# Kernel tuning notes

Measured on AMD Instinct MI355X. Metric: run time of the kernel, lower is better.

The kernel has to match this reference:

```python
import jax, jax.numpy as jnp
import numpy as np

N = 1024
EMB = 128
FC = 512


def setup_inputs() -> dict:
    key = jax.random.key(0)
    ks = jax.random.split(key, 13)
    s = 0.05
    return {
        "x": jax.random.normal(ks[0], (N, 2), jnp.float32),
        "w_rel0": jax.random.normal(ks[1], (EMB, 2), jnp.float32) * s,
        "b_rel0": jax.random.normal(ks[2], (EMB,), jnp.float32) * s,
        "w_root0": jax.random.normal(ks[3], (EMB, 2), jnp.float32) * s,
        "w_rel1": jax.random.normal(ks[4], (EMB, EMB), jnp.float32) * s,
        "b_rel1": jax.random.normal(ks[5], (EMB,), jnp.float32) * s,
        "w_root1": jax.random.normal(ks[6], (EMB, EMB), jnp.float32) * s,
        "lw0": jax.random.normal(ks[7], (FC, EMB), jnp.float32) * s,
        "lb0": jax.random.normal(ks[8], (FC,), jnp.float32) * s,
        "lw1": jax.random.normal(ks[9], (FC, FC), jnp.float32) * s,
        "lb1": jax.random.normal(ks[10], (FC,), jnp.float32) * s,
        "lw2": jax.random.normal(ks[11], (1, FC), jnp.float32) * s,
        "lb2": jax.random.normal(ks[12], (1,), jnp.float32) * s,
    }


def _sage(x, w_rel, b_rel, w_root):
    # DenseSAGEConv with adj = all-ones NxN: neighbor mean == global mean.
    # out = lin_rel(adj@x / deg) + lin_root(x); lin_root has no bias.
    agg = jnp.mean(x, axis=0, keepdims=True)            # (1, d_in)
    return agg @ w_rel.T + b_rel + x @ w_root.T          # (N, d_out)


def reference(x, w_rel0, b_rel0, w_root0, w_rel1, b_rel1, w_root1,
              lw0, lb0, lw1, lb1, lw2, lb2):
    h = jax.nn.relu(_sage(x, w_rel0, b_rel0, w_root0))    # (N, EMB)
    h = jax.nn.relu(_sage(h, w_rel1, b_rel1, w_root1))    # (N, EMB)
    # triu(ones, 1).nonzero() -> all pairs i < j (static, N known at trace time)
    ei, ej = np.triu_indices(h.shape[0], 1)
    e = h[ei] * h[ej]                                     # (E, EMB)
    o = jax.nn.relu(e @ lw0.T + lb0)                      # (E, FC)
    o = jax.nn.relu(o @ lw1.T + lb1)                      # (E, FC)
    o = o @ lw2.T + lb2                                   # (E, 1)
    return jax.nn.sigmoid(o)[:, 0]                        # (E,)
```

## Files before the change

### kernel.cpp

```cpp
#include <hip/hip_runtime.h>
#include <hip/hip_bf16.h>
#include <math.h>

#define NN 1024
#define EMB 128
#define FC 512
#define NEDGE 523776
#define BM 64

typedef __attribute__((ext_vector_type(4))) float f32x4;
typedef __attribute__((ext_vector_type(8))) short bf16x8;
typedef __attribute__((ext_vector_type(4))) unsigned int u32x4;
typedef __attribute__((ext_vector_type(8))) int i32x8;

__device__ __forceinline__ float bf2f(unsigned short u) {
  union { unsigned int i; float f; } v; v.i = ((unsigned int)u) << 16; return v.f;
}
__device__ __forceinline__ unsigned short f2bf(float f) {
  return __builtin_bit_cast(unsigned short, __float2bfloat16(f));
}
__device__ __forceinline__ int cum_edges(int i) { return i * NN - ((i * (i + 1)) >> 1); }

__device__ __forceinline__ unsigned int pk4_fp8(float a, float b, float c, float d) {
  int v = __builtin_amdgcn_cvt_pk_fp8_f32(a, b, 0, false);
  v = __builtin_amdgcn_cvt_pk_fp8_f32(c, d, v, true);
  return (unsigned int)v;
}
#define MFMA_FP8_L0(A,B,C) __builtin_amdgcn_mfma_scale_f32_16x16x128_f8f6f4((A),(B),(C),0,0,0,0x76767676,0,0x7f7f7f7f)
#define MFMA_FP8_L1(A,B,C) __builtin_amdgcn_mfma_scale_f32_16x16x128_f8f6f4((A),(B),(C),0,0,0,0x72727272,0,0x7f7f7f7f)

__global__ void k_cvt_weights(const float* __restrict__ lw0, const float* __restrict__ lw1,
                              unsigned int* __restrict__ w0q, unsigned int* __restrict__ w1q) {
  int d = blockIdx.x * 256 + threadIdx.x;
  if (d < 16384) {
    int dw = d & 7, lane = (d >> 3) & 63, f = (d >> 9) & 3, wv = d >> 11;
    int fc = wv*64 + f*16 + (lane & 15);
    int k  = (lane >> 4)*32 + dw*4;
    float4 s = *(const float4*)(lw0 + fc*EMB + k);
    w0q[d] = pk4_fp8(s.x*64.f, s.y*64.f, s.z*64.f, s.w*64.f);
  } else {
    int u = d - 16384;
    int dw = u & 7, lane = (u >> 3) & 63, f = (u >> 9) & 3, kb = (u >> 11) & 3, wv = u >> 13;
    int fc = wv*64 + f*16 + (lane & 15);
    int k  = kb*128 + (lane >> 4)*32 + dw*4;
    float4 s = *(const float4*)(lw1 + fc*FC + k);
    w1q[u] = pk4_fp8(s.x*64.f, s.y*64.f, s.z*64.f, s.w*64.f);
  }
}

__global__ void k_mean_x(const float* __restrict__ x, float* __restrict__ mean0) {
  __shared__ float sx[256], sy[256];
  float ax = 0.f, ay = 0.f;
  for (int i = threadIdx.x; i < NN; i += 256) { ax += x[2*i]; ay += x[2*i+1]; }
  sx[threadIdx.x] = ax; sy[threadIdx.x] = ay;
  __syncthreads();
  for (int st = 128; st > 0; st >>= 1) {
    if (threadIdx.x < st) { sx[threadIdx.x] += sx[threadIdx.x+st]; sy[threadIdx.x] += sy[threadIdx.x+st]; }
    __syncthreads();
  }
  if (threadIdx.x == 0) { mean0[0] = sx[0] * (1.f/NN); mean0[1] = sy[0] * (1.f/NN); }
}

__global__ void k_sage0(const float* __restrict__ x, const float* __restrict__ wrel,
                        const float* __restrict__ brel, const float* __restrict__ wroot,
                        const float* __restrict__ mean0, float* __restrict__ h0) {
  int idx = blockIdx.x * 256 + threadIdx.x;
  int i = idx >> 7, c = idx & 127;
  float v = mean0[0]*wrel[2*c] + mean0[1]*wrel[2*c+1] + brel[c]
          + x[2*i]*wroot[2*c] + x[2*i+1]*wroot[2*c+1];
  h0[idx] = fmaxf(v, 0.f);
}

__global__ void k_mean_h0(const float* __restrict__ h0, float* __restrict__ mean1) {
  __shared__ float s[256];
  int c = blockIdx.x;
  float a = 0.f;
  for (int i = threadIdx.x; i < NN; i += 256) a += h0[i*EMB + c];
  s[threadIdx.x] = a;
  __syncthreads();
  for (int st = 128; st > 0; st >>= 1) {
    if (threadIdx.x < st) s[threadIdx.x] += s[threadIdx.x+st];
    __syncthreads();
  }
  if (threadIdx.x == 0) mean1[c] = s[0] * (1.f/NN);
}

__global__ void k_relc(const float* __restrict__ mean1, const float* __restrict__ wrel1,
                       const float* __restrict__ brel1, float* __restrict__ relc) {
  int c = threadIdx.x;
  float a = brel1[c];
  #pragma unroll 8
  for (int k = 0; k < EMB; ++k) a += mean1[k] * wrel1[c*EMB + k];
  relc[c] = a;
}

__global__ void k_sage1(const float* __restrict__ h0, const float* __restrict__ wroot1,
                        const float* __restrict__ relc, unsigned short* __restrict__ hb) {
  int idx = blockIdx.x * 256 + threadIdx.x;
  int i = idx >> 7, c = idx & 127;
  const float4* hr = (const float4*)(h0 + i*EMB);
  const float4* wr = (const float4*)(wroot1 + c*EMB);
  float a = relc[c];
  #pragma unroll 8
  for (int k = 0; k < EMB/4; ++k) {
    float4 h = hr[k], w = wr[k];
    a += h.x*w.x + h.y*w.y + h.z*w.z + h.w*w.w;
  }
  hb[idx] = f2bf(fmaxf(a, 0.f) * 32.0f);
}

__global__ __launch_bounds__(512, 4)
void k_edge_mlp(const unsigned short* __restrict__ hb,
                const unsigned int* __restrict__ w0q,
                const float* __restrict__ lb0,
                const unsigned int* __restrict__ w1q,
                const float* __restrict__ lb1,
                const float* __restrict__ lw2,
                const float* __restrict__ lb2,
                float* __restrict__ out) {
  __shared__ __align__(16) unsigned int e_lds[2048];
  __shared__ __align__(16) unsigned int o0_lds[8192];

  const int tid  = threadIdx.x;
  const int lane = tid & 63;
  const int wv   = tid >> 6;
  const int l15  = lane & 15;
  const int l4   = lane >> 4;
  const int blk  = blockIdx.x;
  const int fcb  = wv * 64;

  const char* w0w = (const char*)(w0q + wv * 2048);
  const char* w1w = (const char*)(w1q + wv * 8192);

  {
    int r = tid >> 3, q = tid & 7;
    int k = blk * BM + r;
    float s = sqrtf((float)(4190209 - 8*k));
    int i = (int)((2047.0f - s) * 0.5f);
    if (i < 0) i = 0;
    if (i > NN-2) i = NN-2;
    if (cum_edges(i+1) <= k) ++i;
    if (cum_edges(i+1) <= k) ++i;
    if (cum_edges(i) > k) --i;
    if (cum_edges(i) > k) --i;
    int j = k - cum_edges(i) + i + 1;
    const bf16x8* hi = (const bf16x8*)(hb + i*EMB + q*16);
    const bf16x8* hj = (const bf16x8*)(hb + j*EMB + q*16);
    float p[16];
    #pragma unroll
    for (int g = 0; g < 2; ++g) {
      bf16x8 a = hi[g], b = hj[g];
      #pragma unroll
      for (int u = 0; u < 8; ++u)
        p[g*8+u] = bf2f((unsigned short)a[u]) * bf2f((unsigned short)b[u]);
    }
    u32x4 d;
    #pragma unroll
    for (int u = 0; u < 4; ++u)
      d[u] = pk4_fp8(p[4*u], p[4*u+1], p[4*u+2], p[4*u+3]);
    int byt = (r>>4)*2048 + (q&1)*1024 + ((q>>1)*16 + (r&15))*16;
    *(u32x4*)((char*)e_lds + byt) = d;
  }
  __syncthreads();

  i32x8 a[4];
  #pragma unroll
  for (int f = 0; f < 4; ++f) {
    *(u32x4*)&a[f]       = *(const u32x4*)(w0w + f*2048 + lane*32);
    *((u32x4*)&a[f] + 1) = *(const u32x4*)(w0w + f*2048 + lane*32 + 16);
  }
  f32x4 acc[4][4];
  #pragma unroll
  for (int f = 0; f < 4; ++f) {
    float4 bv = *(const float4*)(lb0 + fcb + f*16 + l4*4);
    #pragma unroll
    for (int e = 0; e < 4; ++e)
      acc[e][f] = (f32x4){bv.x*128.f, bv.y*128.f, bv.z*128.f, bv.w*128.f};
  }
  {
    const char* rbe = (const char*)e_lds + lane*16;
    #pragma unroll
    for (int e = 0; e < 4; ++e) {
      i32x8 b;
      *(u32x4*)&b       = *(const u32x4*)(rbe + e*2048);
      *((u32x4*)&b + 1) = *(const u32x4*)(rbe + e*2048 + 1024);
      __builtin_amdgcn_s_setprio(1);
      #pragma unroll
      for (int f = 0; f < 4; ++f)
        acc[e][f] = MFMA_FP8_L0(a[f], b, acc[e][f]);
      __builtin_amdgcn_s_setprio(0);
    }
  }

  {
    char* ob = (char*)o0_lds + (wv>>1)*2048 + (wv&1)*512 + l15*16 + l4*4;
    #pragma unroll
    for (int f = 0; f < 4; ++f) {
      #pragma unroll
      for (int e = 0; e < 4; ++e) {
        unsigned int d = pk4_fp8(fmaxf(acc[e][f][0], 0.f),
                                 fmaxf(acc[e][f][1], 0.f),
                                 fmaxf(acc[e][f][2], 0.f),
                                 fmaxf(acc[e][f][3], 0.f));
        *(unsigned int*)(ob + e*8192 + (f&1)*1024 + (f>>1)*256) = d;
      }
    }
  }
  __syncthreads();

  #pragma unroll
  for (int f = 0; f < 4; ++f) {
    float4 bv = *(const float4*)(lb1 + fcb + f*16 + l4*4);
    #pragma unroll
    for (int e = 0; e < 4; ++e)
      acc[e][f] = (f32x4){bv.x, bv.y, bv.z, bv.w};
  }
  {
    const char* rbo = (const char*)o0_lds + lane*16;
    #pragma unroll
    for (int kb = 0; kb < 4; ++kb) {
      #pragma unroll
      for (int f = 0; f < 4; ++f) {
        *(u32x4*)&a[f]       = *(const u32x4*)(w1w + kb*8192 + f*2048 + lane*32);
        *((u32x4*)&a[f] + 1) = *(const u32x4*)(w1w + kb*8192 + f*2048 + lane*32 + 16);
      }
      #pragma unroll
      for (int e = 0; e < 4; ++e) {
        i32x8 b;
        *(u32x4*)&b       = *(const u32x4*)(rbo + e*8192 + kb*2048);
        *((u32x4*)&b + 1) = *(const u32x4*)(rbo + e*8192 + kb*2048 + 1024);
        __builtin_amdgcn_s_setprio(1);
        #pragma unroll
        for (int f = 0; f < 4; ++f)
          acc[e][f] = MFMA_FP8_L1(a[f], b, acc[e][f]);
        __builtin_amdgcn_s_setprio(0);
      }
    }
  }

  {
    float rs[4] = {0.f, 0.f, 0.f, 0.f};
    #pragma unroll
    for (int f = 0; f < 4; ++f) {
      float4 l2v = *(const float4*)(lw2 + fcb + f*16 + l4*4);
      #pragma unroll
      for (int e = 0; e < 4; ++e) {
        rs[e] += fmaxf(acc[e][f][0], 0.f) * l2v.x;
        rs[e] += fmaxf(acc[e][f][1], 0.f) * l2v.y;
        rs[e] += fmaxf(acc[e][f][2], 0.f) * l2v.z;
        rs[e] += fmaxf(acc[e][f][3], 0.f) * l2v.w;
      }
    }
    #pragma unroll
    for (int e = 0; e < 4; ++e) {
      rs[e] += __shfl_xor(rs[e], 16, 64);
      rs[e] += __shfl_xor(rs[e], 32, 64);
    }
    float* red = (float*)e_lds;
    if (l4 == 0) {
      #pragma unroll
      for (int e = 0; e < 4; ++e) red[wv*BM + e*16 + l15] = rs[e];
    }
  }
  __syncthreads();

  if (tid < BM) {
    const float* red = (const float*)e_lds;
    float v = lb2[0];
    #pragma unroll
    for (int w = 0; w < 8; ++w) v += red[w*BM + tid];
    out[blk*BM + tid] = 1.0f / (1.0f + __expf(-v));
  }
}

extern "C" void kernel_launch(void* const* d_in, const int* in_sizes, int n_in,
                              void* d_out, int out_size, void* d_ws, size_t ws_size,
                              hipStream_t stream) {
  const float* x      = (const float*)d_in[0];
  const float* wrel0  = (const float*)d_in[1];
  const float* brel0  = (const float*)d_in[2];
  const float* wroot0 = (const float*)d_in[3];
  const float* wrel1  = (const float*)d_in[4];
  const float* brel1  = (const float*)d_in[5];
  const float* wroot1 = (const float*)d_in[6];
  const float* lw0    = (const float*)d_in[7];
  const float* lb0    = (const float*)d_in[8];
  const float* lw1    = (const float*)d_in[9];
  const float* lb1    = (const float*)d_in[10];
  const float* lw2    = (const float*)d_in[11];
  const float* lb2    = (const float*)d_in[12];
  float* out = (float*)d_out;

  char* ws = (char*)d_ws;
  unsigned short* hb  = (unsigned short*)(ws);
  unsigned int*   w0q = (unsigned int*)(ws + 262144);
  unsigned int*   w1q = (unsigned int*)(ws + 327680);
  float* h0    = (float*)(ws + 589824);
  float* mean0 = (float*)(ws + 1114112);
  float* mean1 = (float*)(ws + 1114176);
  float* relc  = (float*)(ws + 1114688);

  hipLaunchKernelGGL(k_cvt_weights, dim3(320), dim3(256), 0, stream, lw0, lw1, w0q, w1q);
  hipLaunchKernelGGL(k_mean_x,   dim3(1),    dim3(256), 0, stream, x, mean0);
  hipLaunchKernelGGL(k_sage0,    dim3(512),  dim3(256), 0, stream, x, wrel0, brel0, wroot0, mean0, h0);
  hipLaunchKernelGGL(k_mean_h0,  dim3(128),  dim3(256), 0, stream, h0, mean1);
  hipLaunchKernelGGL(k_relc,     dim3(1),    dim3(128), 0, stream, mean1, wrel1, brel1, relc);
  hipLaunchKernelGGL(k_sage1,    dim3(512),  dim3(256), 0, stream, h0, wroot1, relc, hb);
  hipLaunchKernelGGL(k_edge_mlp, dim3(NEDGE/BM), dim3(512), 0, stream,
                     hb, w0q, lb0, w1q, lb1, lw2, lb2, out);
}
```

Baseline: 218.2 us.

## Double-buffer layer-1 weight fragments and split edges into two accumulator halves

```diff
diff --git a/kernel.cpp b/kernel.cpp
--- a/kernel.cpp
+++ b/kernel.cpp
@@ -109,6 +109,46 @@
   hb[idx] = f2bf(fmaxf(a, 0.f) * 32.0f);
 }
 
+
+#define L1_PRE(BUF, KB) \
+  { _Pragma("unroll") \
+    for (int f = 0; f < 4; ++f) { \
+      *(u32x4*)&BUF[f]       = *(const u32x4*)(w1w + (KB)*8192 + f*2048 + lane*32); \
+      *((u32x4*)&BUF[f] + 1) = *(const u32x4*)(w1w + (KB)*8192 + f*2048 + lane*32 + 16); \
+    } }
+
+#define L1_MM(BUF, KB, ET0, ET1) \
+  { i32x8 bA, bB; \
+    *(u32x4*)&bA       = *(const u32x4*)(rbo + (ET0)*8192 + (KB)*2048); \
+    *((u32x4*)&bA + 1) = *(const u32x4*)(rbo + (ET0)*8192 + (KB)*2048 + 1024); \
+    *(u32x4*)&bB       = *(const u32x4*)(rbo + (ET1)*8192 + (KB)*2048); \
+    *((u32x4*)&bB + 1) = *(const u32x4*)(rbo + (ET1)*8192 + (KB)*2048 + 1024); \
+    __builtin_amdgcn_s_setprio(1); \
+    _Pragma("unroll") \
+    for (int f = 0; f < 4; ++f) acc1[0][f] = MFMA_FP8_L1(BUF[f], bA, acc1[0][f]); \
+    _Pragma("unroll") \
+    for (int f = 0; f < 4; ++f) acc1[1][f] = MFMA_FP8_L1(BUF[f], bB, acc1[1][f]); \
+    __builtin_amdgcn_s_setprio(0); }
+
+#define L1_EPI(E0, E1) \
+  { float rs0 = 0.f, rs1 = 0.f; \
+    _Pragma("unroll") \
+    for (int f = 0; f < 4; ++f) { \
+      float4 bv  = *(const float4*)(lb1 + fcb + f*16 + l4*4); \
+      float4 wv2 = *(const float4*)(lw2 + fcb + f*16 + l4*4); \
+      rs0 += fmaxf(acc1[0][f][0] + bv.x, 0.f) * wv2.x; \
+      rs0 += fmaxf(acc1[0][f][1] + bv.y, 0.f) * wv2.y; \
+      rs0 += fmaxf(acc1[0][f][2] + bv.z, 0.f) * wv2.z; \
+      rs0 += fmaxf(acc1[0][f][3] + bv.w, 0.f) * wv2.w; \
+      rs1 += fmaxf(acc1[1][f][0] + bv.x, 0.f) * wv2.x; \
+      rs1 += fmaxf(acc1[1][f][1] + bv.y, 0.f) * wv2.y; \
+      rs1 += fmaxf(acc1[1][f][2] + bv.z, 0.f) * wv2.z; \
+      rs1 += fmaxf(acc1[1][f][3] + bv.w, 0.f) * wv2.w; \
+    } \
+    rs0 += __shfl_xor(rs0, 16, 64); rs0 += __shfl_xor(rs0, 32, 64); \
+    rs1 += __shfl_xor(rs1, 16, 64); rs1 += __shfl_xor(rs1, 32, 64); \
+    if (l4 == 0) { red[wv*64 + (E0)*16 + l15] = rs0; red[wv*64 + (E1)*16 + l15] = rs1; } }
+
 __global__ __launch_bounds__(512, 4)
 void k_edge_mlp(const unsigned short* __restrict__ hb,
                 const unsigned int* __restrict__ w0q,
@@ -131,6 +171,16 @@
 
   const char* w0w = (const char*)(w0q + wv * 2048);
   const char* w1w = (const char*)(w1q + wv * 8192);
+
+  i32x8 a0[4], a1[4];
+  #pragma unroll
+  for (int f = 0; f < 4; ++f) {
+    *(u32x4*)&a0[f]       = *(const u32x4*)(w0w + f*2048 + lane*32);
+    *((u32x4*)&a0[f] + 1) = *(const u32x4*)(w0w + f*2048 + lane*32 + 16);
+  }
+  float4 b0v[4];
+  #pragma unroll
+  for (int f = 0; f < 4; ++f) b0v[f] = *(const float4*)(lb0 + fcb + f*16 + l4*4);
 
   {
     int r = tid >> 3, q = tid & 7;
@@ -163,36 +213,30 @@
   }
   __syncthreads();
 
-  i32x8 a[4];
-  #pragma unroll
-  for (int f = 0; f < 4; ++f) {
-    *(u32x4*)&a[f]       = *(const u32x4*)(w0w + f*2048 + lane*32);
-    *((u32x4*)&a[f] + 1) = *(const u32x4*)(w0w + f*2048 + lane*32 + 16);
-  }
-  f32x4 acc[4][4];
-  #pragma unroll
-  for (int f = 0; f < 4; ++f) {
-    float4 bv = *(const float4*)(lb0 + fcb + f*16 + l4*4);
-    #pragma unroll
-    for (int e = 0; e < 4; ++e)
-      acc[e][f] = (f32x4){bv.x*128.f, bv.y*128.f, bv.z*128.f, bv.w*128.f};
-  }
   {
-    const char* rbe = (const char*)e_lds + lane*16;
-    #pragma unroll
-    for (int e = 0; e < 4; ++e) {
-      i32x8 b;
-      *(u32x4*)&b       = *(const u32x4*)(rbe + e*2048);
-      *((u32x4*)&b + 1) = *(const u32x4*)(rbe + e*2048 + 1024);
-      __builtin_amdgcn_s_setprio(1);
+    f32x4 acc[4][4];
+    #pragma unroll
+    for (int f = 0; f < 4; ++f)
       #pragma unroll
-      for (int f = 0; f < 4; ++f)
-        acc[e][f] = MFMA_FP8_L0(a[f], b, acc[e][f]);
-      __builtin_amdgcn_s_setprio(0);
+      for (int e = 0; e < 4; ++e)
+        acc[e][f] = (f32x4){b0v[f].x*128.f, b0v[f].y*128.f, b0v[f].z*128.f, b0v[f].w*128.f};
+    {
+      const char* rbe = (const char*)e_lds + lane*16;
+      #pragma unroll
+      for (int e = 0; e < 4; ++e) {
+        i32x8 b;
+        *(u32x4*)&b       = *(const u32x4*)(rbe + e*2048);
+        *((u32x4*)&b + 1) = *(const u32x4*)(rbe + e*2048 + 1024);
+        __builtin_amdgcn_s_setprio(1);
+        #pragma unroll
+        for (int f = 0; f < 4; ++f)
+          acc[e][f] = MFMA_FP8_L0(a0[f], b, acc[e][f]);
+        __builtin_amdgcn_s_setprio(0);
+      }
     }
-  }
-
-  {
+
+    L1_PRE(a0, 0);
+
     char* ob = (char*)o0_lds + (wv>>1)*2048 + (wv&1)*512 + l15*16 + l4*4;
     #pragma unroll
     for (int f = 0; f < 4; ++f) {
@@ -208,64 +252,34 @@
   }
   __syncthreads();
 
+  const char* rbo = (const char*)o0_lds + lane*16;
+  float* red = (float*)e_lds;
+  f32x4 acc1[2][4];
+
   #pragma unroll
-  for (int f = 0; f < 4; ++f) {
-    float4 bv = *(const float4*)(lb1 + fcb + f*16 + l4*4);
-    #pragma unroll
-    for (int e = 0; e < 4; ++e)
-      acc[e][f] = (f32x4){bv.x, bv.y, bv.z, bv.w};
-  }
-  {
-    const char* rbo = (const char*)o0_lds + lane*16;
-    #pragma unroll
-    for (int kb = 0; kb < 4; ++kb) {
-      #pragma unroll
-      for (int f = 0; f < 4; ++f) {
-        *(u32x4*)&a[f]       = *(const u32x4*)(w1w + kb*8192 + f*2048 + lane*32);
-        *((u32x4*)&a[f] + 1) = *(const u32x4*)(w1w + kb*8192 + f*2048 + lane*32 + 16);
-      }
-      #pragma unroll
-      for (int e = 0; e < 4; ++e) {
-        i32x8 b;
-        *(u32x4*)&b       = *(const u32x4*)(rbo + e*8192 + kb*2048);
-        *((u32x4*)&b + 1) = *(const u32x4*)(rbo + e*8192 + kb*2048 + 1024);
-        __builtin_amdgcn_s_setprio(1);
-        #pragma unroll
-        for (int f = 0; f < 4; ++f)
-          acc[e][f] = MFMA_FP8_L1(a[f], b, acc[e][f]);
-        __builtin_amdgcn_s_setprio(0);
-      }
-    }
-  }
-
-  {
-    float rs[4] = {0.f, 0.f, 0.f, 0.f};
-    #pragma unroll
-    for (int f = 0; f < 4; ++f) {
-      float4 l2v = *(const float4*)(lw2 + fcb + f*16 + l4*4);
-      #pragma unroll
-      for (int e = 0; e < 4; ++e) {
-        rs[e] += fmaxf(acc[e][f][0], 0.f) * l2v.x;
-        rs[e] += fmaxf(acc[e][f][1], 0.f) * l2v.y;
-        rs[e] += fmaxf(acc[e][f][2], 0.f) * l2v.z;
-        rs[e] += fmaxf(acc[e][f][3], 0.f) * l2v.w;
-      }
-    }
-    #pragma unroll
-    for (int e = 0; e < 4; ++e) {
-      rs[e] += __shfl_xor(rs[e], 16, 64);
-      rs[e] += __shfl_xor(rs[e], 32, 64);
-    }
-    float* red = (float*)e_lds;
-    if (l4 == 0) {
-      #pragma unroll
-      for (int e = 0; e < 4; ++e) red[wv*BM + e*16 + l15] = rs[e];
-    }
-  }
+  for (int p = 0; p < 2; ++p)
+    #pragma unroll
+    for (int f = 0; f < 4; ++f)
+      acc1[p][f] = (f32x4){0.f, 0.f, 0.f, 0.f};
+  L1_PRE(a1, 1);  L1_MM(a0, 0, 0, 1);
+  L1_PRE(a0, 2);  L1_MM(a1, 1, 0, 1);
+  L1_PRE(a1, 3);  L1_MM(a0, 2, 0, 1);
+                  L1_MM(a1, 3, 0, 1);
+  L1_EPI(0, 1);
+
+  #pragma unroll
+  for (int p = 0; p < 2; ++p)
+    #pragma unroll
+    for (int f = 0; f < 4; ++f)
+      acc1[p][f] = (f32x4){0.f, 0.f, 0.f, 0.f};
+  L1_PRE(a0, 2);  L1_MM(a1, 3, 2, 3);
+  L1_PRE(a1, 1);  L1_MM(a0, 2, 2, 3);
+  L1_PRE(a0, 0);  L1_MM(a1, 1, 2, 3);
+                  L1_MM(a0, 0, 2, 3);
+  L1_EPI(2, 3);
   __syncthreads();
 
   if (tid < BM) {
-    const float* red = (const float*)e_lds;
     float v = lb2[0];
     #pragma unroll
     for (int w = 0; w < 8; ++w) v += red[w*BM + tid];
```

Result: slower. 357.7 us (+63.9%).

## Switch edge MLP from 16x16x128 to 32x32x64 FP8 scaled MFMA tiles

Applied to the files above, without the earlier changes.

```diff
diff --git a/kernel.cpp b/kernel.cpp
--- a/kernel.cpp
+++ b/kernel.cpp
@@ -8,7 +8,7 @@
 #define NEDGE 523776
 #define BM 64
 
-typedef __attribute__((ext_vector_type(4))) float f32x4;
+typedef __attribute__((ext_vector_type(16))) float f32x16;
 typedef __attribute__((ext_vector_type(8))) short bf16x8;
 typedef __attribute__((ext_vector_type(4))) unsigned int u32x4;
 typedef __attribute__((ext_vector_type(8))) int i32x8;
@@ -26,23 +26,23 @@
   v = __builtin_amdgcn_cvt_pk_fp8_f32(c, d, v, true);
   return (unsigned int)v;
 }
-#define MFMA_FP8_L0(A,B,C) __builtin_amdgcn_mfma_scale_f32_16x16x128_f8f6f4((A),(B),(C),0,0,0,0x76767676,0,0x7f7f7f7f)
-#define MFMA_FP8_L1(A,B,C) __builtin_amdgcn_mfma_scale_f32_16x16x128_f8f6f4((A),(B),(C),0,0,0,0x72727272,0,0x7f7f7f7f)
+#define MFMA32_L0(A,B,C) __builtin_amdgcn_mfma_scale_f32_32x32x64_f8f6f4((A),(B),(C),0,0,0,0x76767676,0,0x7f7f7f7f)
+#define MFMA32_L1(A,B,C) __builtin_amdgcn_mfma_scale_f32_32x32x64_f8f6f4((A),(B),(C),0,0,0,0x72727272,0,0x7f7f7f7f)
 
 __global__ void k_cvt_weights(const float* __restrict__ lw0, const float* __restrict__ lw1,
                               unsigned int* __restrict__ w0q, unsigned int* __restrict__ w1q) {
   int d = blockIdx.x * 256 + threadIdx.x;
   if (d < 16384) {
-    int dw = d & 7, lane = (d >> 3) & 63, f = (d >> 9) & 3, wv = d >> 11;
-    int fc = wv*64 + f*16 + (lane & 15);
-    int k  = (lane >> 4)*32 + dw*4;
+    int dw = d & 7, lane = (d >> 3) & 63, f = (d >> 9) & 1, kb = (d >> 10) & 1, wv = (d >> 11) & 7;
+    int fc = wv*64 + f*32 + (lane & 31);
+    int k  = kb*64 + (lane >> 5)*32 + dw*4;
     float4 s = *(const float4*)(lw0 + fc*EMB + k);
     w0q[d] = pk4_fp8(s.x*64.f, s.y*64.f, s.z*64.f, s.w*64.f);
   } else {
     int u = d - 16384;
-    int dw = u & 7, lane = (u >> 3) & 63, f = (u >> 9) & 3, kb = (u >> 11) & 3, wv = u >> 13;
-    int fc = wv*64 + f*16 + (lane & 15);
-    int k  = kb*128 + (lane >> 4)*32 + dw*4;
+    int dw = u & 7, lane = (u >> 3) & 63, f = (u >> 9) & 1, kb = (u >> 10) & 7, wv = (u >> 13) & 7;
+    int fc = wv*64 + f*32 + (lane & 31);
+    int k  = kb*64 + (lane >> 5)*32 + dw*4;
     float4 s = *(const float4*)(lw1 + fc*FC + k);
     w1q[u] = pk4_fp8(s.x*64.f, s.y*64.f, s.z*64.f, s.w*64.f);
   }
@@ -118,19 +118,19 @@
                 const float* __restrict__ lw2,
                 const float* __restrict__ lb2,
                 float* __restrict__ out) {
-  __shared__ __align__(16) unsigned int e_lds[2048];
-  __shared__ __align__(16) unsigned int o0_lds[8192];
+  __shared__ __align__(32) unsigned int e_lds[2048];
+  __shared__ __align__(32) unsigned int o0_lds[8192];
 
   const int tid  = threadIdx.x;
   const int lane = tid & 63;
   const int wv   = tid >> 6;
-  const int l15  = lane & 15;
-  const int l4   = lane >> 4;
+  const int l31  = lane & 31;
+  const int hi   = lane >> 5;
   const int blk  = blockIdx.x;
   const int fcb  = wv * 64;
 
-  const char* w0w = (const char*)(w0q + wv * 2048);
-  const char* w1w = (const char*)(w1q + wv * 8192);
+  const char* w0w = (const char*)w0q + wv * 8192;
+  const char* w1w = (const char*)w1q + wv * 32768;
 
   {
     int r = tid >> 3, q = tid & 7;
@@ -144,12 +144,12 @@
     if (cum_edges(i) > k) --i;
     if (cum_edges(i) > k) --i;
     int j = k - cum_edges(i) + i + 1;
-    const bf16x8* hi = (const bf16x8*)(hb + i*EMB + q*16);
-    const bf16x8* hj = (const bf16x8*)(hb + j*EMB + q*16);
+    const bf16x8* hi8 = (const bf16x8*)(hb + i*EMB + q*16);
+    const bf16x8* hj8 = (const bf16x8*)(hb + j*EMB + q*16);
     float p[16];
     #pragma unroll
     for (int g = 0; g < 2; ++g) {
-      bf16x8 a = hi[g], b = hj[g];
+      bf16x8 a = hi8[g], b = hj8[g];
       #pragma unroll
       for (int u = 0; u < 8; ++u)
         p[g*8+u] = bf2f((unsigned short)a[u]) * bf2f((unsigned short)b[u]);
@@ -158,108 +158,108 @@
     #pragma unroll
     for (int u = 0; u < 4; ++u)
       d[u] = pk4_fp8(p[4*u], p[4*u+1], p[4*u+2], p[4*u+3]);
-    int byt = (r>>4)*2048 + (q&1)*1024 + ((q>>1)*16 + (r&15))*16;
+    int byt = (r>>5)*4096 + (q>>2)*2048 + ((q>>1)&1)*1024 + (r&31)*32 + (q&1)*16;
     *(u32x4*)((char*)e_lds + byt) = d;
   }
   __syncthreads();
 
-  i32x8 a[4];
+  f32x16 acc[2][2];
+
   #pragma unroll
-  for (int f = 0; f < 4; ++f) {
-    *(u32x4*)&a[f]       = *(const u32x4*)(w0w + f*2048 + lane*32);
-    *((u32x4*)&a[f] + 1) = *(const u32x4*)(w0w + f*2048 + lane*32 + 16);
-  }
-  f32x4 acc[4][4];
+  for (int f = 0; f < 2; ++f)
+    #pragma unroll
+    for (int t = 0; t < 4; ++t) {
+      float4 bv = *(const float4*)(lb0 + fcb + f*32 + t*8 + hi*4);
+      #pragma unroll
+      for (int e = 0; e < 2; ++e) {
+        acc[e][f][4*t+0] = bv.x*128.f; acc[e][f][4*t+1] = bv.y*128.f;
+        acc[e][f][4*t+2] = bv.z*128.f; acc[e][f][4*t+3] = bv.w*128.f;
+      }
+    }
+  {
+    const char* rbe = (const char*)e_lds + lane*32;
+    #pragma unroll
+    for (int kb = 0; kb < 2; ++kb) {
+      i32x8 a0 = *(const i32x8*)(w0w + (kb*2+0)*2048 + lane*32);
+      i32x8 a1 = *(const i32x8*)(w0w + (kb*2+1)*2048 + lane*32);
+      i32x8 b0 = *(const i32x8*)(rbe + kb*2048);
+      i32x8 b1 = *(const i32x8*)(rbe + 4096 + kb*2048);
+      __builtin_amdgcn_s_setprio(1);
+      acc[0][0] = MFMA32_L0(a0, b0, acc[0][0]);
+      acc[0][1] = MFMA32_L0(a1, b0, acc[0][1]);
+      acc[1][0] = MFMA32_L0(a0, b1, acc[1][0]);
+      acc[1][1] = MFMA32_L0(a1, b1, acc[1][1]);
+      __builtin_amdgcn_s_setprio(0);
+    }
+  }
+
+  {
+    char* ob = (char*)o0_lds + wv*2048 + l31*32 + hi*4;
+    #pragma unroll
+    for (int f = 0; f < 2; ++f)
+      #pragma unroll
+      for (int e = 0; e < 2; ++e)
+        #pragma unroll
+        for (int t = 0; t < 4; ++t) {
+          unsigned int d = pk4_fp8(fmaxf(acc[e][f][4*t+0], 0.f),
+                                   fmaxf(acc[e][f][4*t+1], 0.f),
+                                   fmaxf(acc[e][f][4*t+2], 0.f),
+                                   fmaxf(acc[e][f][4*t+3], 0.f));
+          *(unsigned int*)(ob + e*16384 + f*1024 + t*8) = d;
+        }
+  }
+  __syncthreads();
+
   #pragma unroll
-  for (int f = 0; f < 4; ++f) {
-    float4 bv = *(const float4*)(lb0 + fcb + f*16 + l4*4);
-    #pragma unroll
-    for (int e = 0; e < 4; ++e)
-      acc[e][f] = (f32x4){bv.x*128.f, bv.y*128.f, bv.z*128.f, bv.w*128.f};
-  }
-  {
-    const char* rbe = (const char*)e_lds + lane*16;
-    #pragma unroll
-    for (int e = 0; e < 4; ++e) {
-      i32x8 b;
-      *(u32x4*)&b       = *(const u32x4*)(rbe + e*2048);
-      *((u32x4*)&b + 1) = *(const u32x4*)(rbe + e*2048 + 1024);
+  for (int f = 0; f < 2; ++f)
+    #pragma unroll
+    for (int t = 0; t < 4; ++t) {
+      float4 bv = *(const float4*)(lb1 + fcb + f*32 + t*8 + hi*4);
+      #pragma unroll
+      for (int e = 0; e < 2; ++e) {
+        acc[e][f][4*t+0] = bv.x; acc[e][f][4*t+1] = bv.y;
+        acc[e][f][4*t+2] = bv.z; acc[e][f][4*t+3] = bv.w;
+      }
+    }
+  {
+    const char* rbo = (const char*)o0_lds + lane*32;
+    #pragma unroll
+    for (int kb = 0; kb < 8; ++kb) {
+      i32x8 a0 = *(const i32x8*)(w1w + (kb*2+0)*2048 + lane*32);
+      i32x8 a1 = *(const i32x8*)(w1w + (kb*2+1)*2048 + lane*32);
+      i32x8 b0 = *(const i32x8*)(rbo + kb*2048);
+      i32x8 b1 = *(const i32x8*)(rbo + 16384 + kb*2048);
       __builtin_amdgcn_s_setprio(1);
-      #pragma unroll
-      for (int f = 0; f < 4; ++f)
-        acc[e][f] = MFMA_FP8_L0(a[f], b, acc[e][f]);
+      acc[0][0] = MFMA32_L1(a0, b0, acc[0][0]);
+      acc[0][1] = MFMA32_L1(a1, b0, acc[0][1]);
+      acc[1][0] = MFMA32_L1(a0, b1, acc[1][0]);
+      acc[1][1] = MFMA32_L1(a1, b1, acc[1][1]);
       __builtin_amdgcn_s_setprio(0);
     }
   }
 
   {
-    char* ob = (char*)o0_lds + (wv>>1)*2048 + (wv&1)*512 + l15*16 + l4*4;
-    #pragma unroll
-    for (int f = 0; f < 4; ++f) {
-      #pragma unroll
-      for (int e = 0; e < 4; ++e) {
-        unsigned int d = pk4_fp8(fmaxf(acc[e][f][0], 0.f),
-                                 fmaxf(acc[e][f][1], 0.f),
-                                 fmaxf(acc[e][f][2], 0.f),
-                                 fmaxf(acc[e][f][3], 0.f));
-        *(unsigned int*)(ob + e*8192 + (f&1)*1024 + (f>>1)*256) = d;
+    float rs0 = 0.f, rs1 = 0.f;
+    #pragma unroll
+    for (int f = 0; f < 2; ++f)
+      #pragma unroll
+      for (int t = 0; t < 4; ++t) {
+        float4 l2v = *(const float4*)(lw2 + fcb + f*32 + t*8 + hi*4);
+        rs0 += fmaxf(acc[0][f][4*t+0], 0.f) * l2v.x;
+        rs0 += fmaxf(acc[0][f][4*t+1], 0.f) * l2v.y;
+        rs0 += fmaxf(acc[0][f][4*t+2], 0.f) * l2v.z;
+        rs0 += fmaxf(acc[0][f][4*t+3], 0.f) * l2v.w;
+        rs1 += fmaxf(acc[1][f][4*t+0], 0.f) * l2v.x;
+        rs1 += fmaxf(acc[1][f][4*t+1], 0.f) * l2v.y;
+        rs1 += fmaxf(acc[1][f][4*t+2], 0.f) * l2v.z;
+        rs1 += fmaxf(acc[1][f][4*t+3], 0.f) * l2v.w;
       }
-    }
-  }
-  __syncthreads();
-
-  #pragma unroll
-  for (int f = 0; f < 4; ++f) {
-    float4 bv = *(const float4*)(lb1 + fcb + f*16 + l4*4);
-    #pragma unroll
-    for (int e = 0; e < 4; ++e)
-      acc[e][f] = (f32x4){bv.x, bv.y, bv.z, bv.w};
-  }
-  {
-    const char* rbo = (const char*)o0_lds + lane*16;
-    #pragma unroll
-    for (int kb = 0; kb < 4; ++kb) {
-      #pragma unroll
-      for (int f = 0; f < 4; ++f) {
-        *(u32x4*)&a[f]       = *(const u32x4*)(w1w + kb*8192 + f*2048 + lane*32);
-        *((u32x4*)&a[f] + 1) = *(const u32x4*)(w1w + kb*8192 + f*2048 + lane*32 + 16);
-      }
-      #pragma unroll
-      for (int e = 0; e < 4; ++e) {
-        i32x8 b;
-        *(u32x4*)&b       = *(const u32x4*)(rbo + e*8192 + kb*2048);
-        *((u32x4*)&b + 1) = *(const u32x4*)(rbo + e*8192 + kb*2048 + 1024);
-        __builtin_amdgcn_s_setprio(1);
-        #pragma unroll
-        for (int f = 0; f < 4; ++f)
-          acc[e][f] = MFMA_FP8_L1(a[f], b, acc[e][f]);
-        __builtin_amdgcn_s_setprio(0);
-      }
-    }
-  }
-
-  {
-    float rs[4] = {0.f, 0.f, 0.f, 0.f};
-    #pragma unroll
-    for (int f = 0; f < 4; ++f) {
-      float4 l2v = *(const float4*)(lw2 + fcb + f*16 + l4*4);
-      #pragma unroll
-      for (int e = 0; e < 4; ++e) {
-        rs[e] += fmaxf(acc[e][f][0], 0.f) * l2v.x;
-        rs[e] += fmaxf(acc[e][f][1], 0.f) * l2v.y;
-        rs[e] += fmaxf(acc[e][f][2], 0.f) * l2v.z;
-        rs[e] += fmaxf(acc[e][f][3], 0.f) * l2v.w;
-      }
-    }
-    #pragma unroll
-    for (int e = 0; e < 4; ++e) {
-      rs[e] += __shfl_xor(rs[e], 16, 64);
-      rs[e] += __shfl_xor(rs[e], 32, 64);
-    }
+    rs0 += __shfl_xor(rs0, 32, 64);
+    rs1 += __shfl_xor(rs1, 32, 64);
     float* red = (float*)e_lds;
-    if (l4 == 0) {
-      #pragma unroll
-      for (int e = 0; e < 4; ++e) red[wv*BM + e*16 + l15] = rs[e];
+    if (hi == 0) {
+      red[wv*64 + l31]      = rs0;
+      red[wv*64 + 32 + l31] = rs1;
     }
   }
   __syncthreads();
```

Result: faster. 198.9 us (-8.9%).
